# Optimization experiments

Measured on AMD Instinct MI355X. Metric: run time of the kernel, lower is better.

## Reference

```python
import jax, jax.numpy as jnp
import numpy as np


def setup_inputs() -> dict:
    key = jax.random.key(0)
    k1, k2, k3, k4, k5 = jax.random.split(key, 5)
    B, L1, L2, H = 16, 1024, 1024, 1024
    x = jax.random.normal(k1, (B, L1, H), dtype=jnp.float32)
    y = jax.random.normal(k2, (B, L2, H), dtype=jnp.float32)
    y_mask = jax.random.randint(k3, (B, L2), 0, 2) > 0  # True = masked out
    W = jax.random.normal(k4, (H, H), dtype=jnp.float32) * (1.0 / np.sqrt(H))
    b = jax.random.normal(k5, (H,), dtype=jnp.float32) * 0.01
    return {"x": x, "y": y, "y_mask": y_mask, "W": W, "b": b}


def reference(x, y, y_mask, W, b):
    # shared linear projection + ReLU (nn.Linear: v @ W.T + b)
    x_proj = jax.nn.relu(jnp.einsum("blh,dh->bld", x, W) + b)  # [B, L1, H]
    y_proj = jax.nn.relu(jnp.einsum("bmh,dh->bmd", y, W) + b)  # [B, L2, H]
    # unscaled attention scores [B, L1, L2]
    scores = jnp.einsum("bld,bmd->blm", x_proj, y_proj)
    scores = jnp.where(y_mask[:, None, :], -jnp.inf, scores)
    alpha = jax.nn.softmax(scores, axis=-1)
    # weighted sum over original (unprojected) y values
    matched_seq = jnp.einsum("blm,bmh->blh", alpha, y)
    return matched_seq
```

## Files before the change

kernel.cpp:

```cpp
#include <hip/hip_runtime.h>
#include <hip/hip_fp16.h>

typedef _Float16 f16;
typedef _Float16 half4 __attribute__((ext_vector_type(4)));
typedef _Float16 half8 __attribute__((ext_vector_type(8)));
typedef float f32x4 __attribute__((ext_vector_type(4)));

#define BATCH 16
#define L 1024
#define H 1024

__global__ __launch_bounds__(256) void prep(const float* __restrict__ W,
                                            f16* __restrict__ Wh,
                                            const float* __restrict__ x,
                                            f16* __restrict__ Xh,
                                            const int* __restrict__ mask,
                                            int* __restrict__ posx,
                                            int* __restrict__ cntA,
                                            int* __restrict__ tileCtr) {
  __shared__ int wsum[4];
  const int t = threadIdx.x;
  if (blockIdx.x < 8704) {
    const float* src;
    f16* dst;
    long i;
    if (blockIdx.x < 512) {
      src = W; dst = Wh;
      i = (long)blockIdx.x * 2048 + t * 8;
    } else {
      src = x; dst = Xh;
      i = ((long)blockIdx.x - 512) * 2048 + t * 8;
    }
    const float4 a = *(const float4*)(&src[i]);
    const float4 b = *(const float4*)(&src[i + 4]);
    half8 h;
    h[0] = (f16)a.x; h[1] = (f16)a.y; h[2] = (f16)a.z; h[3] = (f16)a.w;
    h[4] = (f16)b.x; h[5] = (f16)b.y; h[6] = (f16)b.z; h[7] = (f16)b.w;
    *(half8*)(&dst[i]) = h;
    return;
  }
  const int b = blockIdx.x - 8704;
  if (b == 0 && t == 0) tileCtr[0] = 0;
  const int4 mk = *(const int4*)(&mask[b * 1024 + t * 4]);
  const int f0 = (mk.x == 0), f1 = (mk.y == 0);
  const int f2 = (mk.z == 0), f3 = (mk.w == 0);
  const int s = f0 + f1 + f2 + f3;
  int v = s;
  const int lane = t & 63, wd = t >> 6;
  #pragma unroll
  for (int off = 1; off < 64; off <<= 1) {
    const int u = __shfl_up(v, off);
    if (lane >= off) v += u;
  }
  if (lane == 63) wsum[wd] = v;
  __syncthreads();
  int wb = 0;
  #pragma unroll
  for (int k = 0; k < 3; ++k)
    if (k < wd) wb += wsum[k];
  int e = wb + v - s;
  const int base = b * 1024 + t * 4;
  posx[base + 0] = e; e += f0;
  posx[base + 1] = e; e += f1;
  posx[base + 2] = e; e += f2;
  posx[base + 3] = e; e += f3;
  if (t == 255) cntA[b] = e;
}

__global__ __launch_bounds__(256) void transpose_y(
    const float* __restrict__ Y, const int* __restrict__ mask,
    const int* __restrict__ posx, const int* __restrict__ cntA,
    f16* __restrict__ Yhc, f16* __restrict__ Ytc) {
  __shared__ f16 tile[64][36];
  __shared__ int cmap[32];
  const int b = blockIdx.z;
  const int h0 = blockIdx.x * 64, m0 = blockIdx.y * 32;
  const int tid = threadIdx.x;
  const float* Yb = Y + (long)b * L * H;
  f16* Ytb = Ytc + (long)b * L * H;

  int rowbase = 0;
  #pragma unroll
  for (int k = 0; k < 16; ++k)
    if (k < b) rowbase += cntA[k];
  const int jbase = posx[b * 1024 + m0];
  const int cnt = cntA[b];
  const int nloc = ((m0 == L - 32) ? cnt : posx[b * 1024 + m0 + 32]) - jbase;

  const int hc = (tid & 15) * 4;
  #pragma unroll
  for (int rr = 0; rr < 2; ++rr) {
    const int m = (tid >> 4) + rr * 16;
    const int gm = b * 1024 + m0 + m;
    const int jc = posx[gm];
    const int un = (mask[gm] == 0);
    const float4 v = *(const float4*)(&Yb[(long)(m0 + m) * H + h0 + hc]);
    half4 h4;
    h4[0] = (f16)v.x; h4[1] = (f16)v.y; h4[2] = (f16)v.z; h4[3] = (f16)v.w;
    tile[hc + 0][m] = h4[0];
    tile[hc + 1][m] = h4[1];
    tile[hc + 2][m] = h4[2];
    tile[hc + 3][m] = h4[3];
    if (un) {
      *(half4*)(&Yhc[(long)(rowbase + jc) * H + h0 + hc]) = h4;
      if (hc == 0) cmap[jc - jbase] = m;
    }
  }
  __syncthreads();
  {
    const int c = tid & 31;
    if (c < nloc) {
      const int m = cmap[c];
      for (int hh = tid >> 5; hh < 64; hh += 8)
        Ytb[(long)(h0 + hh) * L + jbase + c] = tile[hh][m];
    }
  }
  if (m0 == L - 32) {
    const int p = ((cnt + 31) & ~31) - cnt;
    const int c = tid & 31;
    if (c < p)
      for (int hh = tid >> 5; hh < 64; hh += 8)
        Ytb[(long)(h0 + hh) * L + cnt + c] = (f16)0.f;
  }
}

#define GLD16(g, l)                                           \
  __builtin_amdgcn_global_load_lds(                           \
      (const __attribute__((address_space(1))) void*)(g),     \
      (__attribute__((address_space(3))) void*)(l), 16, 0, 0)

#define GEMM_PIPELINE(NTv)                                                   \
  f32x4 acc[4][4];                                                           \
  _Pragma("unroll") for (int i = 0; i < 4; ++i)                              \
      _Pragma("unroll") for (int j = 0; j < 4; ++j)                          \
          acc[i][j] = (f32x4){0.f, 0.f, 0.f, 0.f};                           \
  _Pragma("unroll") for (int p = 0; p < 2; ++p) {                            \
    char* sb = ldsw + p * 24576;                                             \
    GLD16(gA0, sb + wid * 2048);                                             \
    GLD16(gA1, sb + wid * 2048 + 1024);                                      \
    GLD16(gB0, sb + 16384 + wid * 1024);                                     \
    gA0 += 32; gA1 += 32; gB0 += 32;                                         \
  }                                                                          \
  asm volatile("s_waitcnt vmcnt(3)" ::: "memory");                           \
  __builtin_amdgcn_s_barrier();                                              \
  __builtin_amdgcn_sched_barrier(0);                                         \
  int cb = 0, pb = 2 * 24576;                                                \
  for (int t = 0; t < NTv; ++t) {                                            \
    if (t + 2 < NTv) {                                                       \
      char* sb = ldsw + pb;                                                  \
      GLD16(gA0, sb + wid * 2048);                                           \
      GLD16(gA1, sb + wid * 2048 + 1024);                                    \
      GLD16(gB0, sb + 16384 + wid * 1024);                                   \
      gA0 += 32; gA1 += 32; gB0 += 32;                                       \
    }                                                                        \
    const char* base = ldsr + cb;                                            \
    half8 av[4], bv[4];                                                      \
    _Pragma("unroll") for (int j = 0; j < 4; ++j)                            \
        bv[j] = *(const half8*)(base + 16384 + bByte + j * 1024);            \
    _Pragma("unroll") for (int i = 0; i < 4; ++i)                            \
        av[i] = *(const half8*)(base + aByte + i * 1024);                    \
    __builtin_amdgcn_s_setprio(1);                                           \
    _Pragma("unroll") for (int i = 0; i < 4; ++i)                            \
        _Pragma("unroll") for (int j = 0; j < 4; ++j)                        \
            acc[i][j] = __builtin_amdgcn_mfma_f32_16x16x32_f16(              \
                av[i], bv[j], acc[i][j], 0, 0, 0);                           \
    __builtin_amdgcn_s_setprio(0);                                           \
    if (t < NTv - 1) {                                                       \
      __builtin_amdgcn_sched_barrier(0);                                     \
      if (t <= NTv - 3)                                                      \
        asm volatile("s_waitcnt vmcnt(3)" ::: "memory");                     \
      else                                                                   \
        asm volatile("s_waitcnt vmcnt(0)" ::: "memory");                     \
      __builtin_amdgcn_s_barrier();                                          \
      __builtin_amdgcn_sched_barrier(0);                                     \
      cb = (cb == 49152) ? 0 : cb + 24576;                                   \
      pb = (pb == 49152) ? 0 : pb + 24576;                                   \
    }                                                                        \
  }

__global__ __launch_bounds__(512, 4) void gemm_proj(
    const f16* __restrict__ Ap, const f16* __restrict__ Wp,
    const float* __restrict__ bias, f16* __restrict__ Cp,
    const int* __restrict__ cntA, int* __restrict__ tileCtr) {
  __shared__ f16 lds[3 * 12288];
  __shared__ int sTile;
  constexpr int N = 1024, K = 1024;
  const int tid = threadIdx.x;
  const int lane = tid & 63;
  const int wid = tid >> 6;
  const int wm = wid >> 1, wn = wid & 1;
  int total = 0;
  #pragma unroll
  for (int k = 0; k < 16; ++k) total += cntA[k];
  const int Ntiles = ((16384 + total + 32 + 255) >> 8) << 3;

  const int srow = lane >> 2;
  const int sslot = (lane & 3) ^ ((lane >> 3) & 3);
  const int fr = lane & 15, fq = lane >> 4;
  const int rsw = (fq ^ ((fr >> 1) & 3)) << 4;
  const int aByte = (wm * 64 + fr) * 64 + rsw;
  const int bByte = (wn * 64 + fr) * 64 + rsw;
  char* ldsw = (char*)lds;
  const char* ldsr = (const char*)lds;

  while (true) {
    if (tid == 0) sTile = atomicAdd(tileCtr, 1);
    __syncthreads();
    const int tile = sTile;
    if (tile >= Ntiles) return;
    const int row0 = (tile >> 3) * 256, col0 = (tile & 7) * 128;
    const f16* gA0 = Ap + (long)(row0 + wid * 32 + srow) * K + sslot * 8;
    const f16* gA1 = gA0 + 16L * K;
    const f16* gB0 = Wp + (long)(col0 + wid * 16 + srow) * K + sslot * 8;

    GEMM_PIPELINE(32)

    f16* C = Cp;
    #pragma unroll
    for (int j = 0; j < 4; ++j) {
      const int col = col0 + wn * 64 + j * 16 + fr;
      const float bvs = bias[col];
      #pragma unroll
      for (int i = 0; i < 4; ++i) {
        const int rowb = row0 + wm * 64 + i * 16 + fq * 4;
        #pragma unroll
        for (int r = 0; r < 4; ++r) {
          float v = acc[i][j][r] + bvs;
          v = v > 0.f ? v : 0.f;
          C[(long)(rowb + r) * N + col] = (f16)v;
        }
      }
    }
    __syncthreads();
  }
}

template <int MODE>
__global__ __launch_bounds__(512, 4) void gemm128(
    const f16* __restrict__ Ap, const f16* __restrict__ Bp,
    void* __restrict__ Cp, const int* __restrict__ cntA) {
  __shared__ f16 lds[3 * 12288];
  constexpr int N = 1024, K = 1024;
  const int tid = threadIdx.x;
  const int lane = tid & 63;
  const int wid = tid >> 6;
  const int wm = wid >> 1, wn = wid & 1;

  const int nwg = gridDim.x;
  const int orig = blockIdx.x;
  const int wg = (orig & 7) * (nwg >> 3) + (orig >> 3);
  const int bz = wg >> 5;
  const int rxy = wg & 31;
  const int bx = rxy & 7;
  const int by = rxy >> 3;
  const int row0 = by * 256, col0 = bx * 128;

  int off = 0;
  #pragma unroll
  for (int k = 0; k < 16; ++k)
    if (k < bz) off += cntA[k];
  const int cnt = cntA[bz];
  const int cnt32 = (cnt + 31) & ~31;

  const int srow = lane >> 2;
  const int sslot = (lane & 3) ^ ((lane >> 3) & 3);

  int nt = 32;
  const f16 *gA0, *gA1, *gB0;
  if (MODE == 1) {
    if (col0 >= cnt32) return;
    gA0 = Ap + (long)(bz * 1024 + row0 + wid * 32 + srow) * K + sslot * 8;
    gA1 = gA0 + 16L * K;
    gB0 = Ap + (long)(16384 + off + col0 + wid * 16 + srow) * K + sslot * 8;
  } else {
    nt = cnt32 >> 5;
    gA0 = Ap + (long)bz * (1 << 20) +
          (long)(row0 + wid * 32 + srow) * 1024 + sslot * 8;
    gA1 = gA0 + 16L * 1024;
    gB0 = Bp + (long)bz * (1 << 20) +
          (long)(col0 + wid * 16 + srow) * 1024 + sslot * 8;
  }
  char* ldsw = (char*)lds;

  const int fr = lane & 15, fq = lane >> 4;
  const int rsw = (fq ^ ((fr >> 1) & 3)) << 4;
  const int aByte = (wm * 64 + fr) * 64 + rsw;
  const int bByte = (wn * 64 + fr) * 64 + rsw;
  const char* ldsr = (const char*)lds;

  const int NT = (MODE == 2) ? nt : 32;
  GEMM_PIPELINE(NT)

  float* C = (float*)Cp + (long)bz * (1 << 20);
  #pragma unroll
  for (int j = 0; j < 4; ++j) {
    const int col = col0 + wn * 64 + j * 16 + fr;
    #pragma unroll
    for (int i = 0; i < 4; ++i) {
      const int rowb = row0 + wm * 64 + i * 16 + fq * 4;
      #pragma unroll
      for (int r = 0; r < 4; ++r)
        C[(long)(rowb + r) * N + col] = acc[i][j][r];
    }
  }
}

__global__ __launch_bounds__(256) void softmax_rows(const float* __restrict__ S,
                                                    const int* __restrict__ cntA,
                                                    f16* __restrict__ P) {
  const int b = blockIdx.y;
  const int l = blockIdx.x;
  const int t = threadIdx.x;
  const int cnt = cntA[b];
  const int cnt32 = (cnt + 31) & ~31;
  const float* srow = S + ((long)b * L + l) * L;
  f16* prow = P + ((long)b * L + l) * L;

  const int j0 = t * 4;
  float4 v = make_float4(-1e30f, -1e30f, -1e30f, -1e30f);
  if (j0 < cnt32) v = *(const float4*)(&srow[j0]);
  const float x0 = (j0 + 0 < cnt) ? v.x : -1e30f;
  const float x1 = (j0 + 1 < cnt) ? v.y : -1e30f;
  const float x2 = (j0 + 2 < cnt) ? v.z : -1e30f;
  const float x3 = (j0 + 3 < cnt) ? v.w : -1e30f;

  float mx = fmaxf(fmaxf(x0, x1), fmaxf(x2, x3));
  #pragma unroll
  for (int off = 32; off >= 1; off >>= 1)
    mx = fmaxf(mx, __shfl_xor(mx, off));
  __shared__ float red[8];
  const int wd = t >> 6, lane = t & 63;
  if (lane == 0) red[wd] = mx;
  __syncthreads();
  mx = fmaxf(fmaxf(red[0], red[1]), fmaxf(red[2], red[3]));

  const float e0 = __expf(x0 - mx), e1 = __expf(x1 - mx);
  const float e2 = __expf(x2 - mx), e3 = __expf(x3 - mx);
  float s = e0 + e1 + e2 + e3;
  #pragma unroll
  for (int off = 32; off >= 1; off >>= 1)
    s += __shfl_xor(s, off);
  if (lane == 0) red[4 + wd] = s;
  __syncthreads();
  s = red[4] + red[5] + red[6] + red[7];
  const float inv = 1.f / s;
  if (j0 < cnt32) {
    half4 h;
    h[0] = (f16)(e0 * inv); h[1] = (f16)(e1 * inv);
    h[2] = (f16)(e2 * inv); h[3] = (f16)(e3 * inv);
    *(half4*)(&prow[j0]) = h;
  }
}

extern "C" void kernel_launch(void* const* d_in, const int* in_sizes, int n_in,
                              void* d_out, int out_size, void* d_ws,
                              size_t ws_size, hipStream_t stream) {
  const float* x = (const float*)d_in[0];
  const float* y = (const float*)d_in[1];
  const int* ymask = (const int*)d_in[2];
  const float* W = (const float*)d_in[3];
  const float* bias = (const float*)d_in[4];
  float* out = (float*)d_out;

  char* ws = (char*)d_ws;
  f16* Wh = (f16*)(ws);
  f16* Ytc = (f16*)(ws + (1L << 21));
  f16* XYp = (f16*)(ws + (1L << 21) + (1L << 25));
  f16* XYh = (f16*)(ws + (1L << 21) + (1L << 25) + (1L << 26));
  float* Sc = (float*)XYh;
  f16* Alpha = XYp;

  char* meta = (char*)XYp + 60L * (1 << 20);
  int* posx = (int*)meta;
  int* cntA = (int*)(meta + (1 << 16));
  int* tileCtr = (int*)(meta + (1 << 16) + 256);

  f16* Xh = XYh;
  f16* Yhc = XYh + (long)BATCH * L * H;

  prep<<<8704 + 16, 256, 0, stream>>>(W, Wh, x, Xh, ymask, posx, cntA,
                                      tileCtr);
  transpose_y<<<dim3(16, 32, BATCH), 256, 0, stream>>>(y, ymask, posx, cntA,
                                                       Yhc, Ytc);

  gemm_proj<<<512, 512, 0, stream>>>(XYh, Wh, bias, XYp, cntA, tileCtr);

  gemm128<1><<<512, 512, 0, stream>>>(XYp, nullptr, Sc, cntA);

  softmax_rows<<<dim3(L, BATCH), 256, 0, stream>>>(Sc, cntA, Alpha);

  gemm128<2><<<512, 512, 0, stream>>>(Alpha, Ytc, out, cntA);
}
```

Measured before the change: 205.9 us.

## Replace atomic tile scheduler with static grid and 128-row tiles for Y part

The projection GEMM drops the persistent atomic-counter work queue and launches a static 1536-block grid. Blocks are interleaved between full 256x128 tiles for the X rows and 128x128 tiles for the compacted Y rows. Blocks beyond the unmasked Y count exit early. This removes the atomic and barrier per tile and cuts padding waste on the variable-length Y tail, at the cost of many idle blocks and a second, smaller-tile pipeline with lower per-block reuse.

```diff
diff --git a/kernel.cpp b/kernel.cpp
--- a/kernel.cpp
+++ b/kernel.cpp
@@ -16,8 +16,7 @@
                                             f16* __restrict__ Xh,
                                             const int* __restrict__ mask,
                                             int* __restrict__ posx,
-                                            int* __restrict__ cntA,
-                                            int* __restrict__ tileCtr) {
+                                            int* __restrict__ cntA) {
   __shared__ int wsum[4];
   const int t = threadIdx.x;
   if (blockIdx.x < 8704) {
@@ -40,7 +39,6 @@
     return;
   }
   const int b = blockIdx.x - 8704;
-  if (b == 0 && t == 0) tileCtr[0] = 0;
   const int4 mk = *(const int4*)(&mask[b * 1024 + t * 4]);
   const int f0 = (mk.x == 0), f1 = (mk.y == 0);
   const int f2 = (mk.z == 0), f3 = (mk.w == 0);
@@ -181,41 +179,51 @@
 __global__ __launch_bounds__(512, 4) void gemm_proj(
     const f16* __restrict__ Ap, const f16* __restrict__ Wp,
     const float* __restrict__ bias, f16* __restrict__ Cp,
-    const int* __restrict__ cntA, int* __restrict__ tileCtr) {
+    const int* __restrict__ cntA) {
   __shared__ f16 lds[3 * 12288];
-  __shared__ int sTile;
   constexpr int N = 1024, K = 1024;
   const int tid = threadIdx.x;
   const int lane = tid & 63;
   const int wid = tid >> 6;
-  const int wm = wid >> 1, wn = wid & 1;
+
   int total = 0;
   #pragma unroll
   for (int k = 0; k < 16; ++k) total += cntA[k];
-  const int Ntiles = ((16384 + total + 32 + 255) >> 8) << 3;
+  const int Mh = (total + 127) >> 7;
+
+  const int x = blockIdx.x & 7;
+  const int v = blockIdx.x >> 3;
+  const int Hx = (Mh > x) ? 8 * ((Mh - x + 7) >> 3) : 0;
+  bool full;
+  int k;
+  if (v < 128) {
+    full = !(v & 1);
+    k = v >> 1;
+  } else {
+    full = false;
+    k = v - 64;
+  }
+  if (!full && k >= Hx) return;
 
   const int srow = lane >> 2;
   const int sslot = (lane & 3) ^ ((lane >> 3) & 3);
   const int fr = lane & 15, fq = lane >> 4;
   const int rsw = (fq ^ ((fr >> 1) & 3)) << 4;
-  const int aByte = (wm * 64 + fr) * 64 + rsw;
-  const int bByte = (wn * 64 + fr) * 64 + rsw;
   char* ldsw = (char*)lds;
   const char* ldsr = (const char*)lds;
 
-  while (true) {
-    if (tid == 0) sTile = atomicAdd(tileCtr, 1);
-    __syncthreads();
-    const int tile = sTile;
-    if (tile >= Ntiles) return;
-    const int row0 = (tile >> 3) * 256, col0 = (tile & 7) * 128;
+  if (full) {
+    const int q = x + 8 * (k >> 3);
+    const int row0 = q * 256, col0 = (k & 7) * 128;
+    const int wm = wid >> 1, wn = wid & 1;
+    const int aByte = (wm * 64 + fr) * 64 + rsw;
+    const int bByte = (wn * 64 + fr) * 64 + rsw;
     const f16* gA0 = Ap + (long)(row0 + wid * 32 + srow) * K + sslot * 8;
     const f16* gA1 = gA0 + 16L * K;
     const f16* gB0 = Wp + (long)(col0 + wid * 16 + srow) * K + sslot * 8;
 
     GEMM_PIPELINE(32)
 
-    f16* C = Cp;
     #pragma unroll
     for (int j = 0; j < 4; ++j) {
       const int col = col0 + wn * 64 + j * 16 + fr;
@@ -225,13 +233,88 @@
         const int rowb = row0 + wm * 64 + i * 16 + fq * 4;
         #pragma unroll
         for (int r = 0; r < 4; ++r) {
-          float v = acc[i][j][r] + bvs;
-          v = v > 0.f ? v : 0.f;
-          C[(long)(rowb + r) * N + col] = (f16)v;
+          float vv = acc[i][j][r] + bvs;
+          vv = vv > 0.f ? vv : 0.f;
+          Cp[(long)(rowb + r) * N + col] = (f16)vv;
         }
       }
     }
-    __syncthreads();
+  } else {
+    const int p = x + 8 * (k >> 3);
+    const int row0 = 16384 + p * 128, col0 = (k & 7) * 128;
+    const int wm2 = wid >> 2, wn2 = wid & 3;
+    const int aByte = (wm2 * 64 + fr) * 64 + rsw;
+    const int bByte = (wn2 * 32 + fr) * 64 + rsw;
+    const f16* gA0 = Ap + (long)(row0 + wid * 16 + srow) * K + sslot * 8;
+    const f16* gB0 = Wp + (long)(col0 + wid * 16 + srow) * K + sslot * 8;
+
+    f32x4 acc[4][2];
+    #pragma unroll
+    for (int i = 0; i < 4; ++i)
+      #pragma unroll
+      for (int j = 0; j < 2; ++j)
+        acc[i][j] = (f32x4){0.f, 0.f, 0.f, 0.f};
+    #pragma unroll
+    for (int p2 = 0; p2 < 2; ++p2) {
+      char* sb = ldsw + p2 * 24576;
+      GLD16(gA0, sb + wid * 1024);
+      GLD16(gB0, sb + 16384 + wid * 1024);
+      gA0 += 32; gB0 += 32;
+    }
+    asm volatile("s_waitcnt vmcnt(2)" ::: "memory");
+    __builtin_amdgcn_s_barrier();
+    __builtin_amdgcn_sched_barrier(0);
+    int cb = 0, pb = 2 * 24576;
+    for (int t = 0; t < 32; ++t) {
+      if (t + 2 < 32) {
+        char* sb = ldsw + pb;
+        GLD16(gA0, sb + wid * 1024);
+        GLD16(gB0, sb + 16384 + wid * 1024);
+        gA0 += 32; gB0 += 32;
+      }
+      const char* base = ldsr + cb;
+      half8 av[4], bv[2];
+      #pragma unroll
+      for (int j = 0; j < 2; ++j)
+        bv[j] = *(const half8*)(base + 16384 + bByte + j * 1024);
+      #pragma unroll
+      for (int i = 0; i < 4; ++i)
+        av[i] = *(const half8*)(base + aByte + i * 1024);
+      __builtin_amdgcn_s_setprio(1);
+      #pragma unroll
+      for (int i = 0; i < 4; ++i)
+        #pragma unroll
+        for (int j = 0; j < 2; ++j)
+          acc[i][j] = __builtin_amdgcn_mfma_f32_16x16x32_f16(av[i], bv[j],
+                                                             acc[i][j], 0, 0, 0);
+      __builtin_amdgcn_s_setprio(0);
+      if (t < 31) {
+        __builtin_amdgcn_sched_barrier(0);
+        if (t <= 29)
+          asm volatile("s_waitcnt vmcnt(2)" ::: "memory");
+        else
+          asm volatile("s_waitcnt vmcnt(0)" ::: "memory");
+        __builtin_amdgcn_s_barrier();
+        __builtin_amdgcn_sched_barrier(0);
+        cb = (cb == 49152) ? 0 : cb + 24576;
+        pb = (pb == 49152) ? 0 : pb + 24576;
+      }
+    }
+    #pragma unroll
+    for (int j = 0; j < 2; ++j) {
+      const int col = col0 + wn2 * 32 + j * 16 + fr;
+      const float bvs = bias[col];
+      #pragma unroll
+      for (int i = 0; i < 4; ++i) {
+        const int rowb = row0 + wm2 * 64 + i * 16 + fq * 4;
+        #pragma unroll
+        for (int r = 0; r < 4; ++r) {
+          float vv = acc[i][j][r] + bvs;
+          vv = vv > 0.f ? vv : 0.f;
+          Cp[(long)(rowb + r) * N + col] = (f16)vv;
+        }
+      }
+    }
   }
 }
 
@@ -373,17 +456,15 @@
   char* meta = (char*)XYp + 60L * (1 << 20);
   int* posx = (int*)meta;
   int* cntA = (int*)(meta + (1 << 16));
-  int* tileCtr = (int*)(meta + (1 << 16) + 256);
 
   f16* Xh = XYh;
   f16* Yhc = XYh + (long)BATCH * L * H;
 
-  prep<<<8704 + 16, 256, 0, stream>>>(W, Wh, x, Xh, ymask, posx, cntA,
-                                      tileCtr);
+  prep<<<8704 + 16, 256, 0, stream>>>(W, Wh, x, Xh, ymask, posx, cntA);
   transpose_y<<<dim3(16, 32, BATCH), 256, 0, stream>>>(y, ymask, posx, cntA,
                                                        Yhc, Ytc);
 
-  gemm_proj<<<512, 512, 0, stream>>>(XYh, Wh, bias, XYp, cntA, tileCtr);
+  gemm_proj<<<1536, 512, 0, stream>>>(XYh, Wh, bias, XYp, cntA);
 
   gemm128<1><<<512, 512, 0, stream>>>(XYp, nullptr, Sc, cntA);
 
```

New measurement: 193.3 us, median of 2. -6.1%, faster.
